# Performance work log

Hardware: AMD Instinct MI355X
Metric: run time of the kernel (lower is better)

The kernel has to match this reference:

```python
import jax, jax.numpy as jnp
import numpy as np

N, H, W = 4096, 96, 96
C0 = 0.28209479177387814
C1 = 0.4886025119029199
C2 = [1.0925484305920792, -1.0925484305920792, 0.31539156525252005, -1.0925484305920792, 0.5462742152960396]
C3 = [-0.5900435899266435, 2.890611442640554, -0.4570457994644658, 0.3731763325901154, -0.4570457994644658, 1.445305721320277, -0.5900435899266435]


def setup_inputs() -> dict:
    key = jax.random.key(0)
    ks = jax.random.split(key, 6)
    return {
        'pws': jax.random.normal(ks[0], (N, 3), jnp.float32),
        'low_shs': 0.5 * jax.random.normal(ks[1], (N, 3), jnp.float32),
        'high_shs': 0.1 * jax.random.normal(ks[2], (N, 45), jnp.float32),
        'alphas_raw': jax.random.normal(ks[3], (N, 1), jnp.float32),
        'scales_raw': 0.5 * jax.random.normal(ks[4], (N, 3), jnp.float32) - 3.0,
        'rots_raw': jax.random.normal(ks[5], (N, 4), jnp.float32),
        'us': jnp.zeros((N, 2), jnp.float32),
        'Rcw': jnp.eye(3, dtype=jnp.float32),
        'tcw': jnp.array([0.0, 0.0, 4.0], jnp.float32),
        'cam_intr': jnp.array([120.0, 120.0, 48.0, 48.0], jnp.float32),  # fx fy cx cy
    }


def quat_to_rot(q):
    w, x, y, z = q[:, 0], q[:, 1], q[:, 2], q[:, 3]
    return jnp.stack([
        jnp.stack([1 - 2 * (y * y + z * z), 2 * (x * y - w * z), 2 * (x * z + w * y)], -1),
        jnp.stack([2 * (x * y + w * z), 1 - 2 * (x * x + z * z), 2 * (y * z - w * x)], -1),
        jnp.stack([2 * (x * z - w * y), 2 * (y * z + w * x), 1 - 2 * (x * x + y * y)], -1),
    ], -2)  # [N,3,3]


def sh2color(shs, dirs):
    # shs [N,16,3], dirs [N,3] normalized view directions
    x, y, z = dirs[:, 0:1], dirs[:, 1:2], dirs[:, 2:3]
    xx, yy, zz = x * x, y * y, z * z
    xy, yz, xz = x * y, y * z, x * z
    c = C0 * shs[:, 0]
    c = c - C1 * y * shs[:, 1] + C1 * z * shs[:, 2] - C1 * x * shs[:, 3]
    c = (c + C2[0] * xy * shs[:, 4] + C2[1] * yz * shs[:, 5]
         + C2[2] * (2 * zz - xx - yy) * shs[:, 6]
         + C2[3] * xz * shs[:, 7] + C2[4] * (xx - yy) * shs[:, 8])
    c = (c + C3[0] * y * (3 * xx - yy) * shs[:, 9] + C3[1] * xy * z * shs[:, 10]
         + C3[2] * y * (4 * zz - xx - yy) * shs[:, 11]
         + C3[3] * z * (2 * zz - 3 * xx - 3 * yy) * shs[:, 12]
         + C3[4] * x * (4 * zz - xx - yy) * shs[:, 13]
         + C3[5] * z * (xx - yy) * shs[:, 14]
         + C3[6] * x * (xx - 3 * yy) * shs[:, 15])
    return jnp.maximum(c + 0.5, 0.0)  # [N,3]


def _forward(pws, low_shs, high_shs, alphas_raw, scales_raw, rots_raw, Rcw, tcw, cam_intr):
    fx, fy, cx, cy = cam_intr[0], cam_intr[1], cam_intr[2], cam_intr[3]
    alphas = jax.nn.sigmoid(alphas_raw)[:, 0]                 # get_alphas
    scales = jnp.exp(scales_raw)                              # get_scales
    rots = rots_raw / jnp.linalg.norm(rots_raw, axis=1, keepdims=True)  # get_rots
    shs = jnp.concatenate([low_shs, high_shs], axis=1).reshape(-1, 16, 3)

    # --- project ---
    pcs = pws @ Rcw.T + tcw                                   # [N,3] camera coords
    depths = pcs[:, 2]
    zs = jnp.where(depths > 1e-6, depths, 1e-6)
    u = jnp.stack([fx * pcs[:, 0] / zs + cx, fy * pcs[:, 1] / zs + cy], axis=1)

    # --- cov3d = (R S)(R S)^T ---
    M = quat_to_rot(rots) * scales[:, None, :]
    cov3d = M @ jnp.swapaxes(M, 1, 2)                          # [N,3,3]

    # --- cov2d = J W cov3d W^T J^T + 0.3 I ---
    limx, limy = 1.3 * (W / (2.0 * fx)), 1.3 * (H / (2.0 * fy))
    tx = jnp.clip(pcs[:, 0] / zs, -limx, limx) * zs
    ty = jnp.clip(pcs[:, 1] / zs, -limy, limy) * zs
    zero = jnp.zeros_like(zs)
    J = jnp.stack([
        jnp.stack([fx / zs, zero, -fx * tx / (zs * zs)], -1),
        jnp.stack([zero, fy / zs, -fy * ty / (zs * zs)], -1),
    ], -2)                                                     # [N,2,3]
    T = J @ Rcw
    cov2d = T @ cov3d @ jnp.swapaxes(T, 1, 2)
    a = cov2d[:, 0, 0] + 0.3
    b = cov2d[:, 0, 1]
    c2 = cov2d[:, 1, 1] + 0.3

    # --- inverseCov2D + areas (radius of 3-sigma ellipse) ---
    det = a * c2 - b * b
    cinv = jnp.stack([c2, -b, a], axis=1) / det[:, None]       # [N,3]
    mid = 0.5 * (a + c2)
    lam = mid + jnp.sqrt(jnp.maximum(mid * mid - det, 0.1))
    radius = jnp.ceil(3.0 * jnp.sqrt(lam))
    areas = jnp.stack([radius, radius], axis=1)                # [N,2]

    # --- sh2Color ---
    twc = -(Rcw.T @ tcw)
    dirs = pws - twc
    dirs = dirs / jnp.linalg.norm(dirs, axis=1, keepdims=True)
    colors = sh2color(shs, dirs)                               # [N,3]

    # --- splat: depth-sorted alpha compositing ---
    valid = depths > 0.2
    order = jnp.argsort(depths)
    u_s, cinv_s = u[order], cinv[order]
    alpha_s, color_s, valid_s = alphas[order], colors[order], valid[order]

    px = (jnp.arange(W, dtype=jnp.float32))[None, :].repeat(H, 0).reshape(-1)
    py = (jnp.arange(H, dtype=jnp.float32))[:, None].repeat(W, 1).reshape(-1)
    dx = u_s[:, 0:1] - px[None, :]                             # [N,P]
    dy = u_s[:, 1:2] - py[None, :]
    power = -0.5 * (cinv_s[:, 0:1] * dx * dx + cinv_s[:, 2:3] * dy * dy) - cinv_s[:, 1:2] * dx * dy
    ap = jnp.minimum(alpha_s[:, None] * jnp.exp(jnp.minimum(power, 0.0)), 0.99)
    ap = jnp.where((ap >= 1.0 / 255.0) & valid_s[:, None], ap, 0.0)
    logt = jnp.cumsum(jnp.log1p(-ap), axis=0)
    tau = jnp.exp(jnp.concatenate([jnp.zeros((1, ap.shape[1])), logt[:-1]], axis=0))
    wgt = jnp.where(tau > 1e-4, ap * tau, 0.0)                 # [N,P]
    image = jnp.einsum('nc,np->cp', color_s, wgt).reshape(3, H, W)
    return image, areas


def reference(pws, low_shs, high_shs, alphas_raw, scales_raw, rots_raw, us, Rcw, tcw, cam_intr):
    return _forward(pws, low_shs, high_shs, alphas_raw, scales_raw, rots_raw, Rcw, tcw, cam_intr)
```

## Files before the change

kernel.cpp:

```cpp
#include <hip/hip_runtime.h>
#include <hip/hip_bf16.h>
#include <math.h>

#define GS_N 4096
#define IMG_H 96
#define IMG_W 96
#define NPIX (IMG_H * IMG_W)
#define TILE_PX 12
#define TILES_X 8
#define NTILES (TILES_X * TILES_X)
#define WAVES_PER_TILE 36

#define SH_C0 0.28209479177387814f
#define SH_C1 0.4886025119029199f
__device__ __constant__ float kC2[5] = {1.0925484305920792f, -1.0925484305920792f, 0.31539156525252005f, -1.0925484305920792f, 0.5462742152960396f};
__device__ __constant__ float kC3[7] = {-0.5900435899266435f, 2.890611442640554f, -0.4570457994644658f, 0.3731763325901154f, -0.4570457994644658f, 1.445305721320277f, -0.5900435899266435f};

__global__ __launch_bounds__(256) void gs_prep(
    const float* __restrict__ pws, const float* __restrict__ low_shs,
    const float* __restrict__ high_shs, const float* __restrict__ alphas_raw,
    const float* __restrict__ scales_raw, const float* __restrict__ rots_raw,
    const float* __restrict__ Rcw, const float* __restrict__ tcw,
    const float* __restrict__ cam,
    float* __restrict__ areas_out,
    float* __restrict__ depth_ws,
    float4* __restrict__ A_uns,
    float4* __restrict__ B_uns,
    float* __restrict__ C_uns,
    float4* __restrict__ D_uns)
{
    int i = blockIdx.x * 256 + threadIdx.x;
    if (i >= GS_N) return;

    float fx = cam[0], fy = cam[1], cxi = cam[2], cyi = cam[3];
    float R0 = Rcw[0], R1 = Rcw[1], R2 = Rcw[2];
    float R3 = Rcw[3], R4 = Rcw[4], R5 = Rcw[5];
    float R6 = Rcw[6], R7 = Rcw[7], R8 = Rcw[8];
    float t0 = tcw[0], t1 = tcw[1], t2 = tcw[2];

    float pwx = pws[3*i+0], pwy = pws[3*i+1], pwz = pws[3*i+2];

    float pcx = R0*pwx + R1*pwy + R2*pwz + t0;
    float pcy = R3*pwx + R4*pwy + R5*pwz + t1;
    float pcz = R6*pwx + R7*pwy + R8*pwz + t2;

    float depth = pcz;
    float zs = (depth > 1e-6f) ? depth : 1e-6f;

    float ux = fx * pcx / zs + cxi;
    float uy = fy * pcy / zs + cyi;

    float alpha = 1.0f / (1.0f + expf(-alphas_raw[i]));

    float s0 = expf(scales_raw[3*i+0]);
    float s1 = expf(scales_raw[3*i+1]);
    float s2 = expf(scales_raw[3*i+2]);

    float qw = rots_raw[4*i+0], qx = rots_raw[4*i+1], qy = rots_raw[4*i+2], qz = rots_raw[4*i+3];
    float qn = sqrtf(qw*qw + qx*qx + qy*qy + qz*qz);
    qw /= qn; qx /= qn; qy /= qn; qz /= qn;

    float r00 = 1.0f - 2.0f*(qy*qy + qz*qz);
    float r01 = 2.0f*(qx*qy - qw*qz);
    float r02 = 2.0f*(qx*qz + qw*qy);
    float r10 = 2.0f*(qx*qy + qw*qz);
    float r11 = 1.0f - 2.0f*(qx*qx + qz*qz);
    float r12 = 2.0f*(qy*qz - qw*qx);
    float r20 = 2.0f*(qx*qz - qw*qy);
    float r21 = 2.0f*(qy*qz + qw*qx);
    float r22 = 1.0f - 2.0f*(qx*qx + qy*qy);

    float m00 = r00*s0, m01 = r01*s1, m02 = r02*s2;
    float m10 = r10*s0, m11 = r11*s1, m12 = r12*s2;
    float m20 = r20*s0, m21 = r21*s1, m22 = r22*s2;

    float V00 = m00*m00 + m01*m01 + m02*m02;
    float V01 = m00*m10 + m01*m11 + m02*m12;
    float V02 = m00*m20 + m01*m21 + m02*m22;
    float V11 = m10*m10 + m11*m11 + m12*m12;
    float V12 = m10*m20 + m11*m21 + m12*m22;
    float V22 = m20*m20 + m21*m21 + m22*m22;

    float limx = 1.3f * ((float)IMG_W / (2.0f * fx));
    float limy = 1.3f * ((float)IMG_H / (2.0f * fy));
    float xzr = pcx / zs, yzr = pcy / zs;
    float txv = fminf(fmaxf(xzr, -limx), limx) * zs;
    float tyv = fminf(fmaxf(yzr, -limy), limy) * zs;

    float J00 = fx / zs, J02 = -fx * txv / (zs * zs);
    float J11 = fy / zs, J12 = -fy * tyv / (zs * zs);

    float T00 = J00*R0 + J02*R6, T01 = J00*R1 + J02*R7, T02 = J00*R2 + J02*R8;
    float T10 = J11*R3 + J12*R6, T11 = J11*R4 + J12*R7, T12 = J11*R5 + J12*R8;

    float TW00 = T00*V00 + T01*V01 + T02*V02;
    float TW01 = T00*V01 + T01*V11 + T02*V12;
    float TW02 = T00*V02 + T01*V12 + T02*V22;
    float TW10 = T10*V00 + T11*V01 + T12*V02;
    float TW11 = T10*V01 + T11*V11 + T12*V12;
    float TW12 = T10*V02 + T11*V12 + T12*V22;

    float c00 = TW00*T00 + TW01*T01 + TW02*T02;
    float c01 = TW00*T10 + TW01*T11 + TW02*T12;
    float c11 = TW10*T10 + TW11*T11 + TW12*T12;

    float a  = c00 + 0.3f;
    float b  = c01;
    float cc = c11 + 0.3f;
    float det = a * cc - b * b;
    float ci0 = cc / det;
    float ci1 = -b / det;
    float ci2 = a / det;

    float mid = 0.5f * (a + cc);
    float lam = mid + sqrtf(fmaxf(mid * mid - det, 0.1f));
    float radius = ceilf(3.0f * sqrtf(lam));
    areas_out[2*i + 0] = radius;
    areas_out[2*i + 1] = radius;

    float twcx = -(R0*t0 + R3*t1 + R6*t2);
    float twcy = -(R1*t0 + R4*t1 + R7*t2);
    float twcz = -(R2*t0 + R5*t1 + R8*t2);
    float dx = pwx - twcx, dy = pwy - twcy, dz = pwz - twcz;
    float dn = sqrtf(dx*dx + dy*dy + dz*dz);
    dx /= dn; dy /= dn; dz /= dn;

    float xx = dx*dx, yy = dy*dy, zz = dz*dz;
    float xy = dx*dy, yz = dy*dz, xz = dx*dz;

    float bas0  = SH_C0;
    float bas1  = -SH_C1 * dy;
    float bas2  =  SH_C1 * dz;
    float bas3  = -SH_C1 * dx;
    float bas4  = kC2[0] * xy;
    float bas5  = kC2[1] * yz;
    float bas6  = kC2[2] * (2.0f*zz - xx - yy);
    float bas7  = kC2[3] * xz;
    float bas8  = kC2[4] * (xx - yy);
    float bas9  = kC3[0] * dy * (3.0f*xx - yy);
    float bas10 = kC3[1] * xy * dz;
    float bas11 = kC3[2] * dy * (4.0f*zz - xx - yy);
    float bas12 = kC3[3] * dz * (2.0f*zz - 3.0f*xx - 3.0f*yy);
    float bas13 = kC3[4] * dx * (4.0f*zz - xx - yy);
    float bas14 = kC3[5] * dz * (xx - yy);
    float bas15 = kC3[6] * dx * (xx - 3.0f*yy);

    float col[3];
    #pragma unroll
    for (int c = 0; c < 3; ++c) {
        const float* hs = high_shs + 45*i + c;
        float acc = bas0 * low_shs[3*i + c];
        acc += bas1  * hs[0*3];
        acc += bas2  * hs[1*3];
        acc += bas3  * hs[2*3];
        acc += bas4  * hs[3*3];
        acc += bas5  * hs[4*3];
        acc += bas6  * hs[5*3];
        acc += bas7  * hs[6*3];
        acc += bas8  * hs[7*3];
        acc += bas9  * hs[8*3];
        acc += bas10 * hs[9*3];
        acc += bas11 * hs[10*3];
        acc += bas12 * hs[11*3];
        acc += bas13 * hs[12*3];
        acc += bas14 * hs[13*3];
        acc += bas15 * hs[14*3];
        col[c] = fmaxf(acc + 0.5f, 0.0f);
    }

    bool valid = depth > 0.2f;
    float al_eff = valid ? alpha : 0.0f;

    float Tthr = __logf(255.0f * al_eff) + 1e-4f;
    float rx = (Tthr > 0.0f) ? sqrtf(2.0f * Tthr * a)  : -1.0f;
    float ry = (Tthr > 0.0f) ? sqrtf(2.0f * Tthr * cc) : -1.0f;

    depth_ws[i] = depth;
    A_uns[i] = make_float4(ux, uy, ci0, ci1);
    B_uns[i] = make_float4(ci2, al_eff, col[0], col[1]);
    C_uns[i] = col[2];
    D_uns[i] = make_float4(ux, uy, rx, ry);
}

__global__ __launch_bounds__(256) void gs_bin_sort(
    const float4* __restrict__ D_uns, const float* __restrict__ depth_ws,
    int* __restrict__ tile_list, int* __restrict__ tile_cnt)
{
    __shared__ __align__(16) float sdep[GS_N + 4];
    __shared__ int   sidx[GS_N];
    __shared__ int s_base;
    __shared__ int warp_off[4];

    int tile = blockIdx.x;
    int tx = tile & (TILES_X - 1), ty = tile >> 3;
    float x0 = (float)(tx * TILE_PX), x1 = (float)(tx * TILE_PX + TILE_PX - 1);
    float y0 = (float)(ty * TILE_PX), y1 = (float)(ty * TILE_PX + TILE_PX - 1);

    int tid = threadIdx.x;
    int lane = tid & 63, w = tid >> 6;
    if (tid == 0) s_base = 0;
    __syncthreads();

    for (int r = 0; r < GS_N / 256; ++r) {
        int g = r * 256 + tid;
        float4 d = D_uns[g];
        bool pred = (d.z >= 0.0f) &&
                    (d.x - d.z <= x1) && (d.x + d.z >= x0) &&
                    (d.y - d.w <= y1) && (d.y + d.w >= y0);
        unsigned long long m = __ballot(pred);
        int before = __popcll(m & ((1ull << lane) - 1ull));
        int wcnt = __popcll(m);
        if (lane == 0) warp_off[w] = wcnt;
        __syncthreads();
        int off = s_base;
        #pragma unroll
        for (int k = 0; k < 4; ++k) if (k < w) off += warp_off[k];
        if (pred) { sdep[off + before] = depth_ws[g]; sidx[off + before] = g; }
        __syncthreads();
        if (tid == 0) s_base += warp_off[0] + warp_off[1] + warp_off[2] + warp_off[3];
    }
    __syncthreads();
    int cnt = s_base;
    if (tid < 4) sdep[cnt + tid] = INFINITY;
    __syncthreads();

    int* list = tile_list + tile * GS_N;
    int cnt4 = (cnt + 3) >> 2;
    const float4* s4 = (const float4*)sdep;
    for (int e = tid; e < cnt; e += 256) {
        float de = sdep[e];
        int rank = 0;
        for (int jj = 0; jj < cnt4; ++jj) {
            float4 v = s4[jj];
            int j0 = jj * 4;
            rank += (v.x < de || (v.x == de && (j0+0) < e)) ? 1 : 0;
            rank += (v.y < de || (v.y == de && (j0+1) < e)) ? 1 : 0;
            rank += (v.z < de || (v.z == de && (j0+2) < e)) ? 1 : 0;
            rank += (v.w < de || (v.w == de && (j0+3) < e)) ? 1 : 0;
        }
        list[rank] = sidx[e];
    }
    if (tid == 0) tile_cnt[tile] = cnt;
}

__global__ __launch_bounds__(256) void gs_raster(
    const float4* __restrict__ A_uns, const float4* __restrict__ B_uns,
    const float* __restrict__ C_uns,
    const int* __restrict__ tile_list, const int* __restrict__ tile_cnt,
    float* __restrict__ img)
{
    int b = blockIdx.x;
    int tile = b / WAVES_PER_TILE;
    int sub  = b - tile * WAVES_PER_TILE;
    int lane = threadIdx.x & 63;
    int wv   = threadIdx.x >> 6;

    int idxp = sub * 4 + wv;
    int lx = idxp % TILE_PX, ly = idxp / TILE_PX;
    int tx = tile & (TILES_X - 1), ty = tile >> 3;
    int pxi = tx * TILE_PX + lx, pyi = ty * TILE_PX + ly;
    float px = (float)pxi, py = (float)pyi;
    int p = pyi * IMG_W + pxi;

    int cnt = tile_cnt[tile];
    const int* list = tile_list + tile * GS_N;

    float carry = 1.0f;
    float accr = 0.0f, accg = 0.0f, accb = 0.0f;

    for (int c0 = 0; c0 < cnt; c0 += 64) {
        int k = c0 + lane;
        float ap = 0.0f, colr = 0.0f, colg = 0.0f, colb = 0.0f;
        if (k < cnt) {
            int n = list[k];
            float4 a4 = A_uns[n];
            float4 b4 = B_uns[n];
            colb = C_uns[n];
            colr = b4.z; colg = b4.w;

            float ddx = a4.x - px;
            float ddy = a4.y - py;
            float pw = -0.5f * (a4.z * ddx * ddx + b4.x * ddy * ddy) - a4.w * ddx * ddy;
            pw = fminf(pw, 0.0f);
            ap = b4.y * __expf(pw);
            ap = fminf(ap, 0.99f);
            ap = (ap >= (1.0f / 255.0f)) ? ap : 0.0f;
        }

        float f = 1.0f - ap;
        float incl = f;
        #pragma unroll
        for (int d = 1; d < 64; d <<= 1) {
            float v = __shfl_up(incl, d, 64);
            if (lane >= d) incl *= v;
        }
        float excl = __shfl_up(incl, 1, 64);
        if (lane == 0) excl = 1.0f;

        float tau = carry * excl;
        float wgt = (tau > 1e-4f) ? ap * tau : 0.0f;
        accr += colr * wgt;
        accg += colg * wgt;
        accb += colb * wgt;

        carry *= __shfl(incl, 63, 64);
        if (carry <= 1e-4f) break;
    }

    #pragma unroll
    for (int d = 32; d >= 1; d >>= 1) {
        accr += __shfl_xor(accr, d, 64);
        accg += __shfl_xor(accg, d, 64);
        accb += __shfl_xor(accb, d, 64);
    }
    if (lane == 0) {
        img[0 * NPIX + p] = accr;
        img[1 * NPIX + p] = accg;
        img[2 * NPIX + p] = accb;
    }
}

extern "C" void kernel_launch(void* const* d_in, const int* in_sizes, int n_in,
                              void* d_out, int out_size, void* d_ws, size_t ws_size,
                              hipStream_t stream) {
    const float* pws        = (const float*)d_in[0];
    const float* low_shs    = (const float*)d_in[1];
    const float* high_shs   = (const float*)d_in[2];
    const float* alphas_raw = (const float*)d_in[3];
    const float* scales_raw = (const float*)d_in[4];
    const float* rots_raw   = (const float*)d_in[5];
    const float* Rcw        = (const float*)d_in[7];
    const float* tcw        = (const float*)d_in[8];
    const float* cam        = (const float*)d_in[9];

    float* out_img   = (float*)d_out;
    float* out_areas = (float*)d_out + 3 * NPIX;

    char* ws = (char*)d_ws;
    float*  depth_ws = (float*) (ws + 0);
    float4* A_uns    = (float4*)(ws + 16384);
    float4* B_uns    = (float4*)(ws + 81920);
    float*  C_uns    = (float*) (ws + 147456);
    float4* D_uns    = (float4*)(ws + 163840);
    int*    tile_cnt = (int*)   (ws + 229376);
    int*    tile_list= (int*)   (ws + 231424);

    gs_prep<<<GS_N / 256, 256, 0, stream>>>(
        pws, low_shs, high_shs, alphas_raw, scales_raw, rots_raw, Rcw, tcw, cam,
        out_areas, depth_ws, A_uns, B_uns, C_uns, D_uns);

    gs_bin_sort<<<NTILES, 256, 0, stream>>>(D_uns, depth_ws, tile_list, tile_cnt);

    gs_raster<<<NTILES * WAVES_PER_TILE, 256, 0, stream>>>(
        A_uns, B_uns, C_uns, tile_list, tile_cnt, out_img);
}
```

Before: 116.2 us.

## Fuse per-tile binning/sort with rasterization into one 1024-thread kernel

Merges the bin-sort and raster kernels into a single kernel. Each of 8 sub-blocks per tile recomputes the tile's culling and rank sort in shared memory, then rasterizes 18 pixels with its 16 waves. This removes one kernel launch and the global tile_list round trip, and widens the sort to 1024 threads. In exchange the sort work is done 8 times per tile instead of once, and only 18 of the 16x2 wave slots per block get a pixel, so 14 waves sit idle on the second pass.

```diff
diff --git a/kernel.cpp b/kernel.cpp
--- a/kernel.cpp
+++ b/kernel.cpp
@@ -1,5 +1,4 @@
 #include <hip/hip_runtime.h>
-#include <hip/hip_bf16.h>
 #include <math.h>
 
 #define GS_N 4096
@@ -9,7 +8,8 @@
 #define TILE_PX 12
 #define TILES_X 8
 #define NTILES (TILES_X * TILES_X)
-#define WAVES_PER_TILE 36
+#define SUBS 8
+#define PIX_PER_SUB 18
 
 #define SH_C0 0.28209479177387814f
 #define SH_C1 0.4886025119029199f
@@ -182,53 +182,61 @@
     D_uns[i] = make_float4(ux, uy, rx, ry);
 }
 
-__global__ __launch_bounds__(256) void gs_bin_sort(
+__global__ __launch_bounds__(1024) void gs_tile(
     const float4* __restrict__ D_uns, const float* __restrict__ depth_ws,
-    int* __restrict__ tile_list, int* __restrict__ tile_cnt)
+    const float4* __restrict__ A_uns, const float4* __restrict__ B_uns,
+    const float* __restrict__ C_uns, float* __restrict__ img)
 {
     __shared__ __align__(16) float sdep[GS_N + 4];
-    __shared__ int   sidx[GS_N];
+    __shared__ int sidx[GS_N];
+    __shared__ int sout[GS_N];
     __shared__ int s_base;
-    __shared__ int warp_off[4];
-
-    int tile = blockIdx.x;
+    __shared__ int warp_off[16];
+
+    int tile = blockIdx.x >> 3;
+    int sub  = blockIdx.x & (SUBS - 1);
     int tx = tile & (TILES_X - 1), ty = tile >> 3;
     float x0 = (float)(tx * TILE_PX), x1 = (float)(tx * TILE_PX + TILE_PX - 1);
     float y0 = (float)(ty * TILE_PX), y1 = (float)(ty * TILE_PX + TILE_PX - 1);
 
-    int tid = threadIdx.x;
+    int tid  = threadIdx.x;
     int lane = tid & 63, w = tid >> 6;
+
     if (tid == 0) s_base = 0;
     __syncthreads();
 
-    for (int r = 0; r < GS_N / 256; ++r) {
-        int g = r * 256 + tid;
+    #pragma unroll
+    for (int r = 0; r < GS_N / 1024; ++r) {
+        int g = r * 1024 + tid;
         float4 d = D_uns[g];
         bool pred = (d.z >= 0.0f) &&
                     (d.x - d.z <= x1) && (d.x + d.z >= x0) &&
                     (d.y - d.w <= y1) && (d.y + d.w >= y0);
         unsigned long long m = __ballot(pred);
         int before = __popcll(m & ((1ull << lane) - 1ull));
-        int wcnt = __popcll(m);
-        if (lane == 0) warp_off[w] = wcnt;
+        if (lane == 0) warp_off[w] = __popcll(m);
         __syncthreads();
-        int off = s_base;
+        int off = s_base, total = 0;
         #pragma unroll
-        for (int k = 0; k < 4; ++k) if (k < w) off += warp_off[k];
+        for (int k = 0; k < 16; ++k) {
+            int v = warp_off[k];
+            total += v;
+            if (k < w) off += v;
+        }
         if (pred) { sdep[off + before] = depth_ws[g]; sidx[off + before] = g; }
         __syncthreads();
-        if (tid == 0) s_base += warp_off[0] + warp_off[1] + warp_off[2] + warp_off[3];
+        if (tid == 0) s_base = s_base + total;
     }
     __syncthreads();
     int cnt = s_base;
     if (tid < 4) sdep[cnt + tid] = INFINITY;
     __syncthreads();
 
-    int* list = tile_list + tile * GS_N;
     int cnt4 = (cnt + 3) >> 2;
     const float4* s4 = (const float4*)sdep;
-    for (int e = tid; e < cnt; e += 256) {
+    for (int e = tid; e < cnt; e += 1024) {
         float de = sdep[e];
+        int ge = sidx[e];
         int rank = 0;
         for (int jj = 0; jj < cnt4; ++jj) {
             float4 v = s4[jj];
@@ -238,85 +246,70 @@
             rank += (v.z < de || (v.z == de && (j0+2) < e)) ? 1 : 0;
             rank += (v.w < de || (v.w == de && (j0+3) < e)) ? 1 : 0;
         }
-        list[rank] = sidx[e];
+        sout[rank] = ge;
     }
-    if (tid == 0) tile_cnt[tile] = cnt;
-}
-
-__global__ __launch_bounds__(256) void gs_raster(
-    const float4* __restrict__ A_uns, const float4* __restrict__ B_uns,
-    const float* __restrict__ C_uns,
-    const int* __restrict__ tile_list, const int* __restrict__ tile_cnt,
-    float* __restrict__ img)
-{
-    int b = blockIdx.x;
-    int tile = b / WAVES_PER_TILE;
-    int sub  = b - tile * WAVES_PER_TILE;
-    int lane = threadIdx.x & 63;
-    int wv   = threadIdx.x >> 6;
-
-    int idxp = sub * 4 + wv;
-    int lx = idxp % TILE_PX, ly = idxp / TILE_PX;
-    int tx = tile & (TILES_X - 1), ty = tile >> 3;
-    int pxi = tx * TILE_PX + lx, pyi = ty * TILE_PX + ly;
-    float px = (float)pxi, py = (float)pyi;
-    int p = pyi * IMG_W + pxi;
-
-    int cnt = tile_cnt[tile];
-    const int* list = tile_list + tile * GS_N;
-
-    float carry = 1.0f;
-    float accr = 0.0f, accg = 0.0f, accb = 0.0f;
-
-    for (int c0 = 0; c0 < cnt; c0 += 64) {
-        int k = c0 + lane;
-        float ap = 0.0f, colr = 0.0f, colg = 0.0f, colb = 0.0f;
-        if (k < cnt) {
-            int n = list[k];
-            float4 a4 = A_uns[n];
-            float4 b4 = B_uns[n];
-            colb = C_uns[n];
-            colr = b4.z; colg = b4.w;
-
-            float ddx = a4.x - px;
-            float ddy = a4.y - py;
-            float pw = -0.5f * (a4.z * ddx * ddx + b4.x * ddy * ddy) - a4.w * ddx * ddy;
-            pw = fminf(pw, 0.0f);
-            ap = b4.y * __expf(pw);
-            ap = fminf(ap, 0.99f);
-            ap = (ap >= (1.0f / 255.0f)) ? ap : 0.0f;
-        }
-
-        float f = 1.0f - ap;
-        float incl = f;
+    __syncthreads();
+
+    for (int ip = w; ip < PIX_PER_SUB; ip += 16) {
+        int idxp = sub * PIX_PER_SUB + ip;
+        int lx = idxp % TILE_PX, ly = idxp / TILE_PX;
+        int pxi = tx * TILE_PX + lx, pyi = ty * TILE_PX + ly;
+        float px = (float)pxi, py = (float)pyi;
+        int p = pyi * IMG_W + pxi;
+
+        float carry = 1.0f;
+        float accr = 0.0f, accg = 0.0f, accb = 0.0f;
+
+        for (int c0 = 0; c0 < cnt; c0 += 64) {
+            int k = c0 + lane;
+            float ap = 0.0f, colr = 0.0f, colg = 0.0f, colb = 0.0f;
+            if (k < cnt) {
+                int n = sout[k];
+                float4 a4 = A_uns[n];
+                float4 b4 = B_uns[n];
+                colb = C_uns[n];
+                colr = b4.z; colg = b4.w;
+
+                float ddx = a4.x - px;
+                float ddy = a4.y - py;
+                float pw = -0.5f * (a4.z * ddx * ddx + b4.x * ddy * ddy) - a4.w * ddx * ddy;
+                pw = fminf(pw, 0.0f);
+                ap = b4.y * __expf(pw);
+                ap = fminf(ap, 0.99f);
+                ap = (ap >= (1.0f / 255.0f)) ? ap : 0.0f;
+            }
+
+            float f = 1.0f - ap;
+            float incl = f;
+            #pragma unroll
+            for (int d = 1; d < 64; d <<= 1) {
+                float v = __shfl_up(incl, d, 64);
+                if (lane >= d) incl *= v;
+            }
+            float excl = __shfl_up(incl, 1, 64);
+            if (lane == 0) excl = 1.0f;
+
+            float tau = carry * excl;
+            float wgt = (tau > 1e-4f) ? ap * tau : 0.0f;
+            accr += colr * wgt;
+            accg += colg * wgt;
+            accb += colb * wgt;
+
+            carry *= __shfl(incl, 63, 64);
+            if (carry <= 1e-4f) break;
+        }
+
         #pragma unroll
-        for (int d = 1; d < 64; d <<= 1) {
-            float v = __shfl_up(incl, d, 64);
-            if (lane >= d) incl *= v;
-        }
-        float excl = __shfl_up(incl, 1, 64);
-        if (lane == 0) excl = 1.0f;
-
-        float tau = carry * excl;
-        float wgt = (tau > 1e-4f) ? ap * tau : 0.0f;
-        accr += colr * wgt;
-        accg += colg * wgt;
-        accb += colb * wgt;
-
-        carry *= __shfl(incl, 63, 64);
-        if (carry <= 1e-4f) break;
-    }
-
-    #pragma unroll
-    for (int d = 32; d >= 1; d >>= 1) {
-        accr += __shfl_xor(accr, d, 64);
-        accg += __shfl_xor(accg, d, 64);
-        accb += __shfl_xor(accb, d, 64);
-    }
-    if (lane == 0) {
-        img[0 * NPIX + p] = accr;
-        img[1 * NPIX + p] = accg;
-        img[2 * NPIX + p] = accb;
+        for (int d = 32; d >= 1; d >>= 1) {
+            accr += __shfl_xor(accr, d, 64);
+            accg += __shfl_xor(accg, d, 64);
+            accb += __shfl_xor(accb, d, 64);
+        }
+        if (lane == 0) {
+            img[0 * NPIX + p] = accr;
+            img[1 * NPIX + p] = accg;
+            img[2 * NPIX + p] = accb;
+        }
     }
 }
 
@@ -342,15 +335,11 @@
     float4* B_uns    = (float4*)(ws + 81920);
     float*  C_uns    = (float*) (ws + 147456);
     float4* D_uns    = (float4*)(ws + 163840);
-    int*    tile_cnt = (int*)   (ws + 229376);
-    int*    tile_list= (int*)   (ws + 231424);
 
     gs_prep<<<GS_N / 256, 256, 0, stream>>>(
         pws, low_shs, high_shs, alphas_raw, scales_raw, rots_raw, Rcw, tcw, cam,
         out_areas, depth_ws, A_uns, B_uns, C_uns, D_uns);
 
-    gs_bin_sort<<<NTILES, 256, 0, stream>>>(D_uns, depth_ws, tile_list, tile_cnt);
-
-    gs_raster<<<NTILES * WAVES_PER_TILE, 256, 0, stream>>>(
-        A_uns, B_uns, C_uns, tile_list, tile_cnt, out_img);
+    gs_tile<<<NTILES * SUBS, 1024, 0, stream>>>(
+        D_uns, depth_ws, A_uns, B_uns, C_uns, out_img);
 }
```

After: 104.6 us. -9.9%, faster.
